# Performance work log

Measured on AMD Instinct MI355X. Metric: run time of the kernel, lower is better.

Reference implementation:

```python
import jax, jax.numpy as jnp
import numpy as np

NN_SIZE = 10  # matches init_kwargs nn_size


def _knn_idx(points, k):
    """points: (B,N,D). Returns (B,N,k) indices of k nearest neighbors, self excluded."""
    sq = jnp.sum(points * points, axis=-1)  # (B,N)
    # squared euclidean distances (B,N,N)
    d2 = sq[:, :, None] + sq[:, None, :] - 2.0 * jnp.einsum('bnd,bmd->bnm', points, points)
    _, idx = jax.lax.top_k(-d2, k + 1)  # smallest distances; first hit is self
    return idx[:, :, 1:]  # drop self -> (B,N,k)


def _uniform_laplacian(points, knn_idx):
    """points: (B,N,D); knn_idx: (B,N,K). lap = mean(neighbors) - point."""
    neigh = jax.vmap(lambda p, i: p[i])(points, knn_idx)  # (B,N,K,D) gather per batch
    return jnp.mean(neigh, axis=2) - points


def setup_inputs() -> dict:
    key = jax.random.key(0)
    k1, k2 = jax.random.split(key)
    B, N, D = 2, 8192, 3
    point1 = jax.random.normal(k1, (B, N, D), dtype=jnp.float32)
    point2 = jax.random.normal(k2, (B, N, D), dtype=jnp.float32)
    return {"point1": point1, "point2": point2}


def reference(point1, point2):
    knn_idx = _knn_idx(point1, NN_SIZE)          # connectivity from ref cloud
    lap1 = _uniform_laplacian(point1, knn_idx)   # (B,N,3)
    lap2 = _uniform_laplacian(point2, knn_idx)   # reuse knn_idx
    # metric = L1Loss (mean reduction); use_norm=False
    return jnp.mean(jnp.abs(lap1 - lap2))
```

## Files before the change

kernel.cpp:

```cpp
#include <hip/hip_runtime.h>
#include <math.h>


constexpr int NPTS  = 8192;
constexpr int NB    = 2;
constexpr int KNN   = 10;
constexpr int QPB   = 64;
constexpr int WPB   = 8;
constexpr int BLOCK = QPB * WPB;
constexpr int MASK13 = 0xFFFFE000;

constexpr int   G    = 32;
constexpr int   NC   = G * G * G;
constexpr float BMIN = -5.5f;
constexpr float BW   = 11.0f;
constexpr float H    = BW / G;
constexpr float INVH = (float)G / BW;

__device__ __forceinline__ void ins1(int l[KNN], int x) {
#pragma unroll
    for (int k = KNN - 1; k > 0; --k) l[k] = min(l[k], max(l[k - 1], x));
    l[0] = min(l[0], x);
}
__device__ __forceinline__ void ins2(int l[KNN], int a, int b) {
    const int b0 = min(a, b), b1 = max(a, b);
#pragma unroll
    for (int k = KNN - 1; k >= 2; --k)
        l[k] = min(l[k], min(max(l[k - 1], b0), max(l[k - 2], b1)));
    l[1] = min(l[1], min(max(l[0], b0), b1));
    l[0] = min(l[0], b0);
}
template<int S>
__device__ __forceinline__ void ins2s(int l[KNN], int a, int b) {
    const int b0 = min(a, b), b1 = max(a, b);
#pragma unroll
    for (int k = KNN - 1; k >= S + 2; --k)
        l[k] = min(l[k], min(max(l[k - 1], b0), max(l[k - 2], b1)));
    l[S + 1] = min(l[S + 1], min(max(l[S], b0), b1));
    l[S] = min(l[S], b0);
}
__device__ __forceinline__ void merge_sorted(int l[KNN], const int p[KNN]) {
    ins2s<0>(l, p[0], p[1]);
    ins2s<2>(l, p[2], p[3]);
    ins2s<4>(l, p[4], p[5]);
    ins2s<6>(l, p[6], p[7]);
    ins2s<8>(l, p[8], p[9]);
}

__global__ void pack_bin(const float* __restrict__ p1, float4* __restrict__ w,
                         int* __restrict__ hist, int* __restrict__ cellof) {
    const int i = blockIdx.x * blockDim.x + threadIdx.x;
    if (i >= NB * NPTS) return;
    const float x = p1[3 * i], y = p1[3 * i + 1], z = p1[3 * i + 2];
    w[i] = make_float4(x, y, z, fmaf(x, x, fmaf(y, y, z * z)));
    const int cx = min(max((int)floorf((x - BMIN) * INVH), 0), G - 1);
    const int cy = min(max((int)floorf((y - BMIN) * INVH), 0), G - 1);
    const int cz = min(max((int)floorf((z - BMIN) * INVH), 0), G - 1);
    const int c = (cz << 10) | (cy << 5) | cx;
    cellof[i] = c;
    atomicAdd(&hist[(i >> 13) * NC + c], 1);
}

__global__ __launch_bounds__(1024)
void scan_cells(const int* __restrict__ hist, int* __restrict__ starts,
                float* __restrict__ out, int* __restrict__ nfail) {
    __shared__ int wsum[16];
    const int b = blockIdx.x, t = threadIdx.x;
    if (b == 0 && t == 0) { out[0] = 0.0f; nfail[0] = 0; }
    const int* hb = hist + b * NC;
    int* sb = starts + b * (NC + 1);
    const int c0 = t * 32;
    int loc[32]; int sum = 0;
#pragma unroll
    for (int j = 0; j < 32; ++j) { loc[j] = hb[c0 + j]; sum += loc[j]; }
    const int lane = t & 63, wv = t >> 6;
    int incl = sum;
#pragma unroll
    for (int off = 1; off < 64; off <<= 1) {
        const int v = __shfl_up(incl, off);
        if (lane >= off) incl += v;
    }
    if (lane == 63) wsum[wv] = incl;
    __syncthreads();
    if (t < 16) {
        const int v = wsum[t];
        int iv = v;
#pragma unroll
        for (int off = 1; off < 16; off <<= 1) {
            const int u = __shfl_up(iv, off);
            if (t >= off) iv += u;
        }
        wsum[t] = iv - v;
    }
    __syncthreads();
    int run = wsum[wv] + incl - sum;
#pragma unroll
    for (int j = 0; j < 32; ++j) { sb[c0 + j] = run; run += loc[j]; }
    if (t == 1023) sb[NC] = run;
}

__global__ void scatter_all(const int* __restrict__ cellof,
                            const int* __restrict__ starts,
                            int* __restrict__ hist,
                            const float4* __restrict__ w,
                            const float* __restrict__ p2,
                            float4* __restrict__ wsorted,
                            float4* __restrict__ p2s) {
    const int i = blockIdx.x * blockDim.x + threadIdx.x;
    if (i >= NB * NPTS) return;
    const int b = i >> 13;
    const int c = cellof[i];
    const int old = atomicSub(&hist[b * NC + c], 1);
    const int pos = b * NPTS + starts[b * (NC + 1) + c] + old - 1;
    wsorted[pos] = w[i];
    p2s[pos] = make_float4(p2[3 * i], p2[3 * i + 1], p2[3 * i + 2], 0.0f);
}

__global__ __launch_bounds__(BLOCK)
void phase1(const float4* __restrict__ wsorted, const float4* __restrict__ p2s,
            const int* __restrict__ starts, float* __restrict__ out,
            int* __restrict__ nfail, int* __restrict__ worklist)
{
    __shared__ int mv[WPB * KNN * QPB];

    const int batch = blockIdx.x >> 7;
    const int lane  = threadIdx.x & 63;
    const int wv    = __builtin_amdgcn_readfirstlane(threadIdx.x >> 6);
    const int qpos  = ((blockIdx.x & 127) << 6) + lane;

    const float4* W  = wsorted + batch * NPTS;
    const float4* P2 = p2s + batch * NPTS;
    const int*    st = starts + batch * (NC + 1);

    const float4 qp = W[qpos];
    const int cx = min(max((int)floorf((qp.x - BMIN) * INVH), 0), G - 1);
    const int cy = min(max((int)floorf((qp.y - BMIN) * INVH), 0), G - 1);
    const int cz = min(max((int)floorf((qp.z - BMIN) * INVH), 0), G - 1);
    const float lox = BMIN + cx * H, loy = BMIN + cy * H, loz = BMIN + cz * H;
    const float df = fminf(fminf(fminf(qp.x - lox, lox + H - qp.x),
                                 fminf(qp.y - loy, loy + H - qp.y)),
                           fminf(qp.z - loz, loz + H - qp.z));
    const float m2x = -2.0f * qp.x, m2y = -2.0f * qp.y, m2z = -2.0f * qp.z;
    const float q2 = qp.w;
    const int IMAX = 0x7FFFFFFF;

    const int s    = (q2 > 4.8f) ? 2 : 1;
    const int runs = (s == 1) ? 9 : 25;

    int l[KNN];
#pragma unroll
    for (int k = 0; k < KNN; ++k) l[k] = IMAX;

    for (int r = 0; r < 25; ++r) {
        if (!__any(r < runs)) break;
        if (r < runs) {
            int dz3 = (r * 86) >> 8;
            const int dy3 = r - 3 * dz3 - 1;  dz3 -= 1;
            int dz5 = (r * 52429) >> 18;
            const int dy5 = r - 5 * dz5 - 2;  dz5 -= 2;
            const int dy = (s == 1) ? dy3 : dy5;
            const int dz = (s == 1) ? dz3 : dz5;
            const int ay = cy + dy, az = cz + dz;
            int j0 = 0, j1 = 0;
            if ((unsigned)ay < G && (unsigned)az < G) {
                const int cbase = (az << 10) | (ay << 5);
                j0 = st[cbase + max(cx - s, 0)];
                j1 = st[cbase + min(cx + s, G - 1) + 1];
            }
            int j = j0 + wv;
            if (j < j1) {
                float4 c4 = W[j];
                while (true) {
                    const int jn = j + WPB;
                    const bool more = jn < j1;
                    float4 nx;
                    if (more) nx = W[jn];
                    const float d2 = fmaf(m2x, c4.x,
                                     fmaf(m2y, c4.y,
                                     fmaf(m2z, c4.z, c4.w + q2)));
                    int key = (__float_as_int(d2) & MASK13) | j;
                    key = (j == qpos) ? IMAX : key;
                    ins1(l, key);
                    if (!more) break;
                    c4 = nx; j = jn;
                }
            }
        }
    }

#pragma unroll
    for (int k = 0; k < KNN; ++k) mv[(wv * KNN + k) * QPB + lane] = l[k];
    __syncthreads();

    if (threadIdx.x < QPB) {
        int M[KNN];
#pragma unroll
        for (int k = 0; k < KNN; ++k) M[k] = IMAX;
#pragma unroll
        for (int e = 0; e < WPB; ++e) {
            int p[KNN];
#pragma unroll
            for (int k = 0; k < KNN; ++k) p[k] = mv[(e * KNN + k) * QPB + lane];
            merge_sorted(M, p);
        }

        const float tau = __int_as_float(M[KNN - 1] & MASK13);
        const float R = (float)s * H + df;
        const bool covered = (tau <= R * R * 0.996f);
        float v = 0.0f;
        if (covered) {
            float s1x = 0, s1y = 0, s1z = 0, s2x = 0, s2y = 0, s2z = 0;
#pragma unroll
            for (int k = 0; k < KNN; ++k) {
                const int j = M[k] & (NPTS - 1);
                const float4 c4 = W[j];
                const float4 n2 = P2[j];
                s1x += c4.x; s1y += c4.y; s1z += c4.z;
                s2x += n2.x; s2y += n2.y; s2z += n2.z;
            }
            const float4 p2v = P2[qpos];
            const float dx = (s1x * 0.1f - qp.x) - (s2x * 0.1f - p2v.x);
            const float dy2 = (s1y * 0.1f - qp.y) - (s2y * 0.1f - p2v.y);
            const float dz2 = (s1z * 0.1f - qp.z) - (s2z * 0.1f - p2v.z);
            v = fabsf(dx) + fabsf(dy2) + fabsf(dz2);
        } else {
            const int wi = atomicAdd(nfail, 1);
            worklist[wi] = (batch << 16) | qpos;
        }
#pragma unroll
        for (int off = 32; off >= 1; off >>= 1) v += __shfl_down(v, off);
        if (threadIdx.x == 0)
            atomicAdd(out, v * (1.0f / (float)(NB * NPTS * 3)));
    }
}

constexpr int P2BLK = 256;
constexpr int P2GRID = 512;

__global__ __launch_bounds__(P2BLK)
void phase2(const float4* __restrict__ wsorted, const float4* __restrict__ p2s,
            const int* __restrict__ nfail, const int* __restrict__ worklist,
            float* __restrict__ out)
{
    const int lane = threadIdx.x & 63;
    const int wv   = threadIdx.x >> 6;
    const int wid  = blockIdx.x * (P2BLK / 64) + wv;
    const int NW   = P2GRID * (P2BLK / 64);
    const int nf   = *nfail;
    const int IMAX = 0x7FFFFFFF;
    float acc = 0.0f;

    for (int i = wid; i < nf; i += NW) {
        const int e = worklist[i];
        const int batch = e >> 16, qpos = e & 0xFFFF;
        const float4* W  = wsorted + batch * NPTS;
        const float4* P2 = p2s + batch * NPTS;
        const float4 qp = W[qpos];
        const float m2x = -2.0f * qp.x, m2y = -2.0f * qp.y, m2z = -2.0f * qp.z;
        const float q2 = qp.w;

        int l[KNN];
#pragma unroll
        for (int k = 0; k < KNN; ++k) l[k] = IMAX;

#pragma unroll 2
        for (int it = 0; it < NPTS / 128; ++it) {
            const int ja = it * 128 + lane, jb = ja + 64;
            const float4 ca = W[ja];
            const float4 cb = W[jb];
            const float da = fmaf(m2x, ca.x, fmaf(m2y, ca.y, fmaf(m2z, ca.z, ca.w + q2)));
            const float db = fmaf(m2x, cb.x, fmaf(m2y, cb.y, fmaf(m2z, cb.z, cb.w + q2)));
            int ka = (__float_as_int(da) & MASK13) | ja;
            int kb = (__float_as_int(db) & MASK13) | jb;
            ka = (ja == qpos) ? IMAX : ka;
            kb = (jb == qpos) ? IMAX : kb;
            ins2(l, ka, kb);
        }
        for (int off = 1; off < 64; off <<= 1) {
            int p[KNN];
#pragma unroll
            for (int k = 0; k < KNN; ++k) p[k] = __shfl_xor(l[k], off);
            merge_sorted(l, p);
        }
        float s1x = 0, s1y = 0, s1z = 0, s2x = 0, s2y = 0, s2z = 0;
#pragma unroll
        for (int k = 0; k < KNN; ++k) {
            const int j = l[k] & (NPTS - 1);
            const float4 c4 = W[j];
            const float4 n2 = P2[j];
            s1x += c4.x; s1y += c4.y; s1z += c4.z;
            s2x += n2.x; s2y += n2.y; s2z += n2.z;
        }
        const float4 p2v = P2[qpos];
        const float dx = (s1x * 0.1f - qp.x) - (s2x * 0.1f - p2v.x);
        const float dy = (s1y * 0.1f - qp.y) - (s2y * 0.1f - p2v.y);
        const float dz = (s1z * 0.1f - qp.z) - (s2z * 0.1f - p2v.z);
        if (lane == 0) acc += fabsf(dx) + fabsf(dy) + fabsf(dz);
    }

    if (lane == 0 && acc != 0.0f)
        atomicAdd(out, acc * (1.0f / (float)(NB * NPTS * 3)));
}

constexpr int CHUNK = NPTS / WPB;

__global__ void prep_pack(const float* __restrict__ p, float4* __restrict__ w) {
    const int i = blockIdx.x * blockDim.x + threadIdx.x;
    if (i < NB * NPTS) {
        const float x = p[3 * i], y = p[3 * i + 1], z = p[3 * i + 2];
        w[i] = make_float4(x, y, z, fmaf(x, x, fmaf(y, y, z * z)));
    }
}

__global__ __launch_bounds__(BLOCK, 2)
void knn_lap(const float4* __restrict__ w1, const float* __restrict__ p2,
             float* __restrict__ out)
{
    __shared__ int mv[WPB * KNN * QPB];
    const int batch = blockIdx.x >> 7;
    const int qbase = (blockIdx.x & 127) << 6;
    const int lane  = threadIdx.x & 63;
    const int wv    = __builtin_amdgcn_readfirstlane(threadIdx.x >> 6);
    const int query = qbase + lane;
    const float4* Wb = w1 + batch * NPTS;
    const float4 qp = Wb[query];
    const float m2x = -2.0f * qp.x, m2y = -2.0f * qp.y, m2z = -2.0f * qp.z;
    const float q2 = qp.w;
    const int IMAX = 0x7FFFFFFF;
    int l[KNN];
#pragma unroll
    for (int k = 0; k < KNN; ++k) l[k] = IMAX;
    const int c0 = wv * CHUNK;
    const float4* cand = Wb + c0;
#pragma unroll 4
    for (int i = 0; i < CHUNK; i += 2) {
        const float4 ca = cand[i];
        const float4 cb = cand[i + 1];
        const int ja = c0 + i, jb = ja + 1;
        const float da = fmaf(m2x, ca.x, fmaf(m2y, ca.y, fmaf(m2z, ca.z, ca.w + q2)));
        const float db = fmaf(m2x, cb.x, fmaf(m2y, cb.y, fmaf(m2z, cb.z, cb.w + q2)));
        int ka = (__float_as_int(da) & MASK13) | ja;
        int kb = (__float_as_int(db) & MASK13) | jb;
        ka = (ja == query) ? IMAX : ka;
        kb = (jb == query) ? IMAX : kb;
        ins2(l, ka, kb);
    }
#pragma unroll
    for (int k = 0; k < KNN; ++k) mv[(wv * KNN + k) * QPB + lane] = l[k];
    __syncthreads();
    if (threadIdx.x < QPB) {
        int m[KNN];
#pragma unroll
        for (int k = 0; k < KNN; ++k) m[k] = IMAX;
#pragma unroll
        for (int e = 0; e < WPB; ++e) {
            int p[KNN];
#pragma unroll
            for (int k = 0; k < KNN; ++k) p[k] = mv[(e * KNN + k) * QPB + lane];
            merge_sorted(m, p);
        }
        const float* P2b = p2 + (size_t)batch * NPTS * 3;
        float s1x = 0, s1y = 0, s1z = 0, s2x = 0, s2y = 0, s2z = 0;
#pragma unroll
        for (int k = 0; k < KNN; ++k) {
            const int j = m[k] & (NPTS - 1);
            const float4 c = Wb[j];
            s1x += c.x; s1y += c.y; s1z += c.z;
            s2x += P2b[3 * j + 0]; s2y += P2b[3 * j + 1]; s2z += P2b[3 * j + 2];
        }
        const int q = qbase + threadIdx.x;
        const float p2x = P2b[3 * q + 0], p2y = P2b[3 * q + 1], p2z = P2b[3 * q + 2];
        const float dx = (s1x * 0.1f - qp.x) - (s2x * 0.1f - p2x);
        const float dy = (s1y * 0.1f - qp.y) - (s2y * 0.1f - p2y);
        const float dz = (s1z * 0.1f - qp.z) - (s2z * 0.1f - p2z);
        float v = fabsf(dx) + fabsf(dy) + fabsf(dz);
#pragma unroll
        for (int off = 32; off >= 1; off >>= 1) v += __shfl_down(v, off);
        if (threadIdx.x == 0)
            atomicAdd(out, v * (1.0f / (float)(NB * NPTS * 3)));
    }
}

extern "C" void kernel_launch(void* const* d_in, const int* in_sizes, int n_in,
                              void* d_out, int out_size, void* d_ws, size_t ws_size,
                              hipStream_t stream) {
    const float* p1 = (const float*)d_in[0];
    const float* p2 = (const float*)d_in[1];
    float* out = (float*)d_out;

    size_t off = 0;
    float4* w       = (float4*)d_ws;               off += (size_t)NB * NPTS * 16;
    int*    hist    = (int*)((char*)d_ws + off);   off += (size_t)NB * NC * 4;
    int*    starts  = (int*)((char*)d_ws + off);   off += (size_t)NB * (NC + 1) * 4 + 8;
    int*    cellof  = (int*)((char*)d_ws + off);   off += (size_t)NB * NPTS * 4;
    float4* wsorted = (float4*)((char*)d_ws + off); off += (size_t)NB * NPTS * 16;
    float4* p2s     = (float4*)((char*)d_ws + off); off += (size_t)NB * NPTS * 16;
    int*    nfail   = (int*)((char*)d_ws + off);   off += 16;
    int*    worklist= (int*)((char*)d_ws + off);   off += (size_t)NB * NPTS * 4;

    if (ws_size < off) {
        hipMemsetAsync(out, 0, sizeof(float), stream);
        prep_pack<<<(NB * NPTS + 255) / 256, 256, 0, stream>>>(p1, w);
        knn_lap<<<NB * (NPTS / QPB), BLOCK, 0, stream>>>(w, p2, out);
        return;
    }

    hipMemsetAsync(hist, 0, (size_t)NB * NC * 4, stream);
    pack_bin<<<(NB * NPTS + 255) / 256, 256, 0, stream>>>(p1, w, hist, cellof);
    scan_cells<<<NB, 1024, 0, stream>>>(hist, starts, out, nfail);
    scatter_all<<<(NB * NPTS + 255) / 256, 256, 0, stream>>>(cellof, starts, hist,
                                                             w, p2, wsorted, p2s);
    phase1<<<NB * (NPTS / QPB), BLOCK, 0, stream>>>(wsorted, p2s, starts, out,
                                                    nfail, worklist);
    phase2<<<P2GRID, P2BLK, 0, stream>>>(wsorted, p2s, nfail, worklist, out);
}
```

Measured before the change: 121.9 us.

## Share wavefront-uniform cell-row scan windows and fuse scan with scatter

Phase1 now checks whether all 64 queries in a wavefront lie in one or two grid rows with a narrow x-span. If so, it scans a shared, scalar-uniform window of neighbouring cells, deduplicating cells common to both rows and processing candidates two at a time with ins2. Otherwise it falls back to the old per-lane variable-radius search. The cell scan and scatter kernels are merged into one kernel, and the output init moves into pack_bin, removing a launch. The tradeoff is that the scatter runs on only two blocks, and the uniform path uses only radius 1, which may push more queries into the phase2 fallback.

```diff
diff --git a/kernel.cpp b/kernel.cpp
--- a/kernel.cpp
+++ b/kernel.cpp
@@ -17,6 +17,8 @@
 constexpr float H    = BW / G;
 constexpr float INVH = (float)G / BW;
 
+__device__ __forceinline__ int iabs(int v) { return v < 0 ? -v : v; }
+
 __device__ __forceinline__ void ins1(int l[KNN], int x) {
 #pragma unroll
     for (int k = KNN - 1; k > 0; --k) l[k] = min(l[k], max(l[k - 1], x));
@@ -48,9 +50,11 @@
 }
 
 __global__ void pack_bin(const float* __restrict__ p1, float4* __restrict__ w,
-                         int* __restrict__ hist, int* __restrict__ cellof) {
+                         int* __restrict__ hist, int* __restrict__ cellof,
+                         float* __restrict__ out, int* __restrict__ nfail) {
     const int i = blockIdx.x * blockDim.x + threadIdx.x;
     if (i >= NB * NPTS) return;
+    if (i == 0) { out[0] = 0.0f; nfail[0] = 0; }
     const float x = p1[3 * i], y = p1[3 * i + 1], z = p1[3 * i + 2];
     w[i] = make_float4(x, y, z, fmaf(x, x, fmaf(y, y, z * z)));
     const int cx = min(max((int)floorf((x - BMIN) * INVH), 0), G - 1);
@@ -62,25 +66,25 @@
 }
 
 __global__ __launch_bounds__(1024)
-void scan_cells(const int* __restrict__ hist, int* __restrict__ starts,
-                float* __restrict__ out, int* __restrict__ nfail) {
+void scan_scatter(int* hist, int* starts, const int* cellof,
+                  const float4* w, const float* p2,
+                  float4* wsorted, float4* p2s) {
     __shared__ int wsum[16];
     const int b = blockIdx.x, t = threadIdx.x;
-    if (b == 0 && t == 0) { out[0] = 0.0f; nfail[0] = 0; }
     const int* hb = hist + b * NC;
     int* sb = starts + b * (NC + 1);
     const int c0 = t * 32;
     int loc[32]; int sum = 0;
 #pragma unroll
     for (int j = 0; j < 32; ++j) { loc[j] = hb[c0 + j]; sum += loc[j]; }
-    const int lane = t & 63, wv = t >> 6;
+    const int lane = t & 63, wvi = t >> 6;
     int incl = sum;
 #pragma unroll
     for (int off = 1; off < 64; off <<= 1) {
         const int v = __shfl_up(incl, off);
         if (lane >= off) incl += v;
     }
-    if (lane == 63) wsum[wv] = incl;
+    if (lane == 63) wsum[wvi] = incl;
     __syncthreads();
     if (t < 16) {
         const int v = wsum[t];
@@ -93,27 +97,20 @@
         wsum[t] = iv - v;
     }
     __syncthreads();
-    int run = wsum[wv] + incl - sum;
+    int run = wsum[wvi] + incl - sum;
 #pragma unroll
     for (int j = 0; j < 32; ++j) { sb[c0 + j] = run; run += loc[j]; }
     if (t == 1023) sb[NC] = run;
-}
-
-__global__ void scatter_all(const int* __restrict__ cellof,
-                            const int* __restrict__ starts,
-                            int* __restrict__ hist,
-                            const float4* __restrict__ w,
-                            const float* __restrict__ p2,
-                            float4* __restrict__ wsorted,
-                            float4* __restrict__ p2s) {
-    const int i = blockIdx.x * blockDim.x + threadIdx.x;
-    if (i >= NB * NPTS) return;
-    const int b = i >> 13;
-    const int c = cellof[i];
-    const int old = atomicSub(&hist[b * NC + c], 1);
-    const int pos = b * NPTS + starts[b * (NC + 1) + c] + old - 1;
-    wsorted[pos] = w[i];
-    p2s[pos] = make_float4(p2[3 * i], p2[3 * i + 1], p2[3 * i + 2], 0.0f);
+    __syncthreads();
+#pragma unroll
+    for (int k = 0; k < NPTS / 1024; ++k) {
+        const int i = b * NPTS + k * 1024 + t;
+        const int c = cellof[i];
+        const int old = atomicSub(&hist[b * NC + c], 1);
+        const int pos = b * NPTS + sb[c] + old - 1;
+        wsorted[pos] = w[i];
+        p2s[pos] = make_float4(p2[3 * i], p2[3 * i + 1], p2[3 * i + 2], 0.0f);
+    }
 }
 
 __global__ __launch_bounds__(BLOCK)
@@ -144,49 +141,131 @@
     const float q2 = qp.w;
     const int IMAX = 0x7FFFFFFF;
 
-    const int s    = (q2 > 4.8f) ? 2 : 1;
-    const int runs = (s == 1) ? 9 : 25;
-
     int l[KNN];
 #pragma unroll
     for (int k = 0; k < KNN; ++k) l[k] = IMAX;
-
-    for (int r = 0; r < 25; ++r) {
-        if (!__any(r < runs)) break;
-        if (r < runs) {
-            int dz3 = (r * 86) >> 8;
-            const int dy3 = r - 3 * dz3 - 1;  dz3 -= 1;
-            int dz5 = (r * 52429) >> 18;
-            const int dy5 = r - 5 * dz5 - 2;  dz5 -= 2;
-            const int dy = (s == 1) ? dy3 : dy5;
-            const int dz = (s == 1) ? dz3 : dz5;
-            const int ay = cy + dy, az = cz + dz;
-            int j0 = 0, j1 = 0;
-            if ((unsigned)ay < G && (unsigned)az < G) {
-                const int cbase = (az << 10) | (ay << 5);
-                j0 = st[cbase + max(cx - s, 0)];
-                j1 = st[cbase + min(cx + s, G - 1) + 1];
-            }
-            int j = j0 + wv;
-            if (j < j1) {
-                float4 c4 = W[j];
-                while (true) {
-                    const int jn = j + WPB;
-                    const bool more = jn < j1;
-                    float4 nx;
-                    if (more) nx = W[jn];
-                    const float d2 = fmaf(m2x, c4.x,
-                                     fmaf(m2y, c4.y,
-                                     fmaf(m2z, c4.z, c4.w + q2)));
-                    int key = (__float_as_int(d2) & MASK13) | j;
-                    key = (j == qpos) ? IMAX : key;
-                    ins1(l, key);
-                    if (!more) break;
-                    c4 = nx; j = jn;
+    int sCov = 1;
+
+    const int rowid = (cz << 5) | cy;
+    int rmin = rowid, rmax = rowid;
+#pragma unroll
+    for (int off = 32; off >= 1; off >>= 1) {
+        rmin = min(rmin, __shfl_xor(rmin, off));
+        rmax = max(rmax, __shfl_xor(rmax, off));
+    }
+    bool two = false;
+    bool uni = (rmax == rmin);
+    if (!uni) {
+        const unsigned long long m0 = __ballot(rowid == rmin);
+        const unsigned long long m1 = __ballot(rowid == rmax);
+        if ((m0 | m1) == 0xFFFFFFFFFFFFFFFFull) { uni = true; two = true; }
+    }
+    if (uni) {
+        int x0mn = (rowid == rmin) ? cx : 999;
+        int x0mx = (rowid == rmin) ? cx : -999;
+        int x1mn = (rowid == rmax) ? cx : 999;
+        int x1mx = (rowid == rmax) ? cx : -999;
+#pragma unroll
+        for (int off = 32; off >= 1; off >>= 1) {
+            x0mn = min(x0mn, __shfl_xor(x0mn, off));
+            x0mx = max(x0mx, __shfl_xor(x0mx, off));
+            x1mn = min(x1mn, __shfl_xor(x1mn, off));
+            x1mx = max(x1mx, __shfl_xor(x1mx, off));
+        }
+        if (x0mx - x0mn > 6 || (two && (x1mx - x1mn > 6))) uni = false;
+        if (uni) {
+            const int gy0 = __builtin_amdgcn_readfirstlane(rmin & 31);
+            const int gz0 = __builtin_amdgcn_readfirstlane(rmin >> 5);
+            const int gy1 = __builtin_amdgcn_readfirstlane(rmax & 31);
+            const int gz1 = __builtin_amdgcn_readfirstlane(rmax >> 5);
+            const int w0lo = __builtin_amdgcn_readfirstlane(max(x0mn - 1, 0));
+            const int w0hi = __builtin_amdgcn_readfirstlane(min(x0mx + 1, G - 1));
+            const int w1lo = __builtin_amdgcn_readfirstlane(max(x1mn - 1, 0));
+            const int w1hi = __builtin_amdgcn_readfirstlane(min(x1mx + 1, G - 1));
+            const int ng = two ? 2 : 1;
+            for (int g = 0; g < ng; ++g) {
+                const int gy = g ? gy1 : gy0, gz = g ? gz1 : gz0;
+                const int oy = g ? gy0 : gy1, oz = g ? gz0 : gz1;
+#pragma unroll
+                for (int dz = -1; dz <= 1; ++dz)
+#pragma unroll
+                for (int dy = -1; dy <= 1; ++dy) {
+                    const int ay = gy + dy, az = gz + dz;
+                    if ((unsigned)ay >= G || (unsigned)az >= G) continue;
+                    const bool cOther = two && (iabs(ay - oy) <= 1) &&
+                                               (iabs(az - oz) <= 1);
+                    if (g == 1 && cOther) continue;
+                    int xlo = g ? w1lo : w0lo;
+                    int xhi = g ? w1hi : w0hi;
+                    if (g == 0 && cOther) { xlo = min(xlo, w1lo); xhi = max(xhi, w1hi); }
+                    const int cbase = (az << 10) | (ay << 5);
+                    const int j0 = __builtin_amdgcn_readfirstlane(st[cbase + xlo]);
+                    const int j1 = __builtin_amdgcn_readfirstlane(st[cbase + xhi + 1]);
+                    int j = j0 + wv;
+                    for (; j + WPB < j1; j += 2 * WPB) {
+                        const float4 ca = W[j];
+                        const float4 cb = W[j + WPB];
+                        const float da = fmaf(m2x, ca.x, fmaf(m2y, ca.y,
+                                         fmaf(m2z, ca.z, ca.w + q2)));
+                        const float db = fmaf(m2x, cb.x, fmaf(m2y, cb.y,
+                                         fmaf(m2z, cb.z, cb.w + q2)));
+                        int ka = (__float_as_int(da) & MASK13) | j;
+                        int kb = (__float_as_int(db) & MASK13) | (j + WPB);
+                        ka = (j == qpos) ? IMAX : ka;
+                        kb = (j + WPB == qpos) ? IMAX : kb;
+                        ins2(l, ka, kb);
+                    }
+                    if (j < j1) {
+                        const float4 ca = W[j];
+                        const float da = fmaf(m2x, ca.x, fmaf(m2y, ca.y,
+                                         fmaf(m2z, ca.z, ca.w + q2)));
+                        int ka = (__float_as_int(da) & MASK13) | j;
+                        ka = (j == qpos) ? IMAX : ka;
+                        ins1(l, ka);
+                    }
                 }
             }
         }
     }
+    if (!uni) {
+        sCov = (q2 > 4.8f) ? 2 : 1;
+        const int runs = (sCov == 1) ? 9 : 25;
+        for (int r = 0; r < 25; ++r) {
+            if (!__any(r < runs)) break;
+            if (r < runs) {
+                int dz3 = (r * 86) >> 8;
+                const int dy3 = r - 3 * dz3 - 1;  dz3 -= 1;
+                int dz5 = (r * 52429) >> 18;
+                const int dy5 = r - 5 * dz5 - 2;  dz5 -= 2;
+                const int dy = (sCov == 1) ? dy3 : dy5;
+                const int dz = (sCov == 1) ? dz3 : dz5;
+                const int ay = cy + dy, az = cz + dz;
+                int j0 = 0, j1 = 0;
+                if ((unsigned)ay < G && (unsigned)az < G) {
+                    const int cbase = (az << 10) | (ay << 5);
+                    j0 = st[cbase + max(cx - sCov, 0)];
+                    j1 = st[cbase + min(cx + sCov, G - 1) + 1];
+                }
+                int j = j0 + wv;
+                if (j < j1) {
+                    float4 c4 = W[j];
+                    while (true) {
+                        const int jn = j + WPB;
+                        const bool more = jn < j1;
+                        float4 nx;
+                        if (more) nx = W[jn];
+                        const float d2 = fmaf(m2x, c4.x, fmaf(m2y, c4.y,
+                                         fmaf(m2z, c4.z, c4.w + q2)));
+                        int key = (__float_as_int(d2) & MASK13) | j;
+                        key = (j == qpos) ? IMAX : key;
+                        ins1(l, key);
+                        if (!more) break;
+                        c4 = nx; j = jn;
+                    }
+                }
+            }
+        }
+    }
 
 #pragma unroll
     for (int k = 0; k < KNN; ++k) mv[(wv * KNN + k) * QPB + lane] = l[k];
@@ -205,7 +284,7 @@
         }
 
         const float tau = __int_as_float(M[KNN - 1] & MASK13);
-        const float R = (float)s * H + df;
+        const float R = (float)sCov * H + df;
         const bool covered = (tau <= R * R * 0.996f);
         float v = 0.0f;
         if (covered) {
@@ -406,10 +485,10 @@
     }
 
     hipMemsetAsync(hist, 0, (size_t)NB * NC * 4, stream);
-    pack_bin<<<(NB * NPTS + 255) / 256, 256, 0, stream>>>(p1, w, hist, cellof);
-    scan_cells<<<NB, 1024, 0, stream>>>(hist, starts, out, nfail);
-    scatter_all<<<(NB * NPTS + 255) / 256, 256, 0, stream>>>(cellof, starts, hist,
-                                                             w, p2, wsorted, p2s);
+    pack_bin<<<(NB * NPTS + 255) / 256, 256, 0, stream>>>(p1, w, hist, cellof,
+                                                          out, nfail);
+    scan_scatter<<<NB, 1024, 0, stream>>>(hist, starts, cellof, w, p2,
+                                          wsorted, p2s);
     phase1<<<NB * (NPTS / QPB), BLOCK, 0, stream>>>(wsorted, p2s, starts, out,
                                                     nfail, worklist);
     phase2<<<P2GRID, P2BLK, 0, stream>>>(wsorted, p2s, nfail, worklist, out);
```

After: 161.0 us. 1.32x slower.
